# Optimization experiments

Measured on AMD Instinct MI355X. Metric: run time of the kernel, lower is better.

The kernel has to match this reference:

```python
import jax, jax.numpy as jnp
import numpy as np

EPS = 1e-5

def _bn(x, gamma, beta):
    # BatchNorm1d forward (batch statistics, biased variance) over node dim
    mu = x.mean(axis=0)
    var = x.var(axis=0)
    return gamma * (x - mu) * jax.lax.rsqrt(var + EPS) + beta

def _gcn_conv(x, W, b, src, dst, n):
    # PyG GCNConv: h = x @ W; symmetric norm with self-loops; scatter-add to dst
    h = x @ W                                   # [N, out]
    ones = jnp.ones(src.shape, dtype=h.dtype)
    deg = jax.ops.segment_sum(ones, dst, num_segments=n) + 1.0  # +1 self-loop
    dinv = jax.lax.rsqrt(deg)                   # deg >= 1 always
    norm = dinv[src] * dinv[dst]                # [E]
    agg = jax.ops.segment_sum(h[src] * norm[:, None], dst, num_segments=n)
    agg = agg + h * (dinv * dinv)[:, None]      # self-loop contribution
    return agg + b

def setup_inputs() -> dict:
    key = jax.random.key(0)
    ks = jax.random.split(key, 10)
    N, E = 100000, 1600000
    Din, Dh, Dout = 256, 128, 128
    e_prev = jax.random.normal(ks[0], (N, Din), dtype=jnp.float32)
    edge_index = jax.random.randint(ks[1], (2, E), 0, N, dtype=jnp.int64)
    proj_W = jax.random.normal(ks[2], (Din, Din), dtype=jnp.float32) * 0.02
    proj_b = jnp.zeros((Din,), dtype=jnp.float32)
    W1 = jax.random.normal(ks[3], (Din, Dh), dtype=jnp.float32) * 0.05
    b1 = jnp.zeros((Dh,), dtype=jnp.float32)
    gamma1 = jnp.ones((Dh,), dtype=jnp.float32)
    beta1 = jnp.zeros((Dh,), dtype=jnp.float32)
    W2 = jax.random.normal(ks[4], (Dh, Dout), dtype=jnp.float32) * 0.05
    b2 = jnp.zeros((Dout,), dtype=jnp.float32)
    gamma2 = jnp.ones((Dout,), dtype=jnp.float32)
    beta2 = jnp.zeros((Dout,), dtype=jnp.float32)
    return {"e_prev": e_prev, "edge_index": edge_index,
            "proj_W": proj_W, "proj_b": proj_b,
            "W1": W1, "b1": b1, "gamma1": gamma1, "beta1": beta1,
            "W2": W2, "b2": b2, "gamma2": gamma2, "beta2": beta2}

def reference(e_prev, edge_index, proj_W, proj_b, W1, b1, gamma1, beta1, W2, b2, gamma2, beta2):
    n = e_prev.shape[0]
    src, dst = edge_index[0], edge_index[1]
    # input_projection (input_dim != hidden_dim branch)
    x = e_prev @ proj_W + proj_b
    x = _gcn_conv(x, W1, b1, src, dst, n)
    x = _bn(x, gamma1, beta1)
    x = jax.nn.relu(x)
    # dropout(0.2) is identity in eval mode
    x = _gcn_conv(x, W2, b2, src, dst, n)
    x = _bn(x, gamma2, beta2)
    return x
```

## Files before the change

### kernel.cpp

```cpp
#include <hip/hip_runtime.h>
#include <hip/hip_bf16.h>
#include <math.h>

#define BN_EPS 1e-5f
#define CAP 6144
#define MAXB 512

typedef __attribute__((ext_vector_type(8))) short short8;
typedef __attribute__((ext_vector_type(4))) float floatx4;

__global__ void init_kernel(int* __restrict__ bcursor, float* __restrict__ stats, int nb) {
    int i = threadIdx.x + blockIdx.x * blockDim.x;
    if (i < nb) bcursor[i] = i * CAP;
    if (i < 1536) stats[i] = 0.0f;
}

__global__ __launch_bounds__(256) void bucket_kernel(
    const int* __restrict__ src, const int* __restrict__ dst,
    int* __restrict__ bcursor, unsigned* __restrict__ buck, int E, int nb)
{
    __shared__ int h[MAXB], resv[MAXB], cur[MAXB];
    for (int t = threadIdx.x; t < nb; t += 256) { h[t] = 0; cur[t] = 0; }
    __syncthreads();
    int per = (E + gridDim.x - 1) / gridDim.x;
    int e0 = blockIdx.x * per;
    int e1 = min(e0 + per, E);
    for (int e = e0 + threadIdx.x; e < e1; e += 256) {
        int d = __builtin_nontemporal_load(&dst[e]);
        atomicAdd(&h[d >> 8], 1);
    }
    __syncthreads();
    for (int t = threadIdx.x; t < nb; t += 256) {
        int c = h[t];
        if (c > 0) resv[t] = atomicAdd(&bcursor[t], c);
    }
    __syncthreads();
    for (int e = e0 + threadIdx.x; e < e1; e += 256) {
        int d = __builtin_nontemporal_load(&dst[e]);
        int s = __builtin_nontemporal_load(&src[e]);
        int b = d >> 8;
        int pos = resv[b] + atomicAdd(&cur[b], 1);
        buck[pos] = ((unsigned)(d & 255) << 17) | (unsigned)s;
    }
}

__global__ void scanB_kernel(const int* __restrict__ bcursor, int* __restrict__ csrBase, int nb) {
    if (threadIdx.x == 0) {
        int run = 0;
        for (int b = 0; b < nb; ++b) {
            csrBase[b] = run;
            run += bcursor[b] - b * CAP;
        }
        csrBase[nb] = run;
    }
}

__global__ __launch_bounds__(256) void csr_kernel(
    const unsigned* __restrict__ buck, const int* __restrict__ bcursor,
    const int* __restrict__ csrBase,
    int* __restrict__ cnt, int* __restrict__ rowptr, float* __restrict__ dinv,
    int* __restrict__ ssrc, int N)
{
    __shared__ int h[256], sc[256], lcur[256];
    int b = blockIdx.x;
    int t = threadIdx.x;
    h[t] = 0;
    __syncthreads();
    int base = b * CAP;
    int nB = bcursor[b] - base;
    for (int i = t; i < nB; i += 256) {
        unsigned v = buck[base + i];
        atomicAdd(&h[v >> 17], 1);
    }
    __syncthreads();
    int myc = h[t];
    sc[t] = myc;
    __syncthreads();
    for (int off = 1; off < 256; off <<= 1) {
        int x = (t >= off) ? sc[t - off] : 0;
        __syncthreads();
        sc[t] += x;
        __syncthreads();
    }
    int ex = sc[t] - myc;
    lcur[t] = ex;
    int node = b * 256 + t;
    int cb = csrBase[b];
    if (node < N) {
        cnt[node]    = myc;
        rowptr[node] = cb + ex;
        dinv[node]   = rsqrtf((float)myc + 1.0f);
    }
    __syncthreads();
    for (int i = t; i < nB; i += 256) {
        unsigned v = buck[base + i];
        int dloc = v >> 17;
        int pos = cb + atomicAdd(&lcur[dloc], 1);
        ssrc[pos] = (int)(v & 0x1FFFFu);
    }
}

__global__ void wcpack_kernel(const float* __restrict__ PW, const float* __restrict__ W1,
                              const float* __restrict__ pb,
                              __hip_bfloat16* __restrict__ Wf1, float* __restrict__ bc) {
    int c = threadIdx.x;
    if (blockIdx.x == 256) {
        float acc = 0.f;
        for (int k = 0; k < 256; ++k) acc = fmaf(pb[k], W1[k * 128 + c], acc);
        bc[c] = acc;
        return;
    }
    int k = blockIdx.x;
    float acc = 0.f;
    for (int kk = 0; kk < 256; ++kk) acc = fmaf(PW[k * 256 + kk], W1[kk * 128 + c], acc);
    int kc = k >> 5, r5 = k & 31, qq = r5 >> 3, j = r5 & 7;
    int ct = c >> 4, l16 = c & 15;
    int lane = qq * 16 + l16;
    Wf1[(((kc * 8 + ct) * 64) + lane) * 8 + j] = __float2bfloat16(acc);
}

template <int K>
__global__ void packW_kernel(const float* __restrict__ W, __hip_bfloat16* __restrict__ Wf) {
    int t = blockIdx.x * 256 + threadIdx.x;
    if (t >= (K / 32) * 8 * 64 * 8) return;
    int j    = t & 7;
    int lane = (t >> 3) & 63;
    int ct   = (t >> 9) & 7;
    int kc   = t >> 12;
    int k = kc * 32 + ((lane >> 4) & 3) * 8 + j;
    int c = ct * 16 + (lane & 15);
    Wf[t] = __float2bfloat16(W[k * 128 + c]);
}

__device__ inline short8 cvt8(float4 a, float4 b) {
    __hip_bfloat162 p0 = __float22bfloat162_rn(make_float2(a.x, a.y));
    __hip_bfloat162 p1 = __float22bfloat162_rn(make_float2(a.z, a.w));
    __hip_bfloat162 p2 = __float22bfloat162_rn(make_float2(b.x, b.y));
    __hip_bfloat162 p3 = __float22bfloat162_rn(make_float2(b.z, b.w));
    union { short8 s; __hip_bfloat162 h[4]; } u;
    u.h[0] = p0; u.h[1] = p1; u.h[2] = p2; u.h[3] = p3;
    return u.s;
}

template <int K, bool BN>
__global__ __launch_bounds__(256) void mfma_gemm(
    const float* __restrict__ X, const short* __restrict__ Wf,
    const float* __restrict__ bias, const float* __restrict__ dinv,
    const float* __restrict__ scale, const float* __restrict__ shift,
    __hip_bfloat16* __restrict__ Hs, int N)
{
    const int wave = threadIdx.x >> 6;
    const int lane = threadIdx.x & 63;
    const int l16  = lane & 15;
    const int q    = lane >> 4;
    const int r0   = blockIdx.x * 128 + wave * 32;

    const int ra0 = min(r0 + l16, N - 1);
    const int ra1 = min(r0 + 16 + l16, N - 1);
    const float* pA0 = X + (size_t)ra0 * K + q * 8;
    const float* pA1 = X + (size_t)ra1 * K + q * 8;
    const short8* WF = (const short8*)Wf;

    floatx4 acc[2][8];
#pragma unroll
    for (int rt = 0; rt < 2; ++rt)
#pragma unroll
        for (int ct = 0; ct < 8; ++ct) { acc[rt][ct][0] = 0.f; acc[rt][ct][1] = 0.f; acc[rt][ct][2] = 0.f; acc[rt][ct][3] = 0.f; }

#pragma unroll
    for (int kc = 0; kc < K / 32; ++kc) {
        short8 b[8];
#pragma unroll
        for (int ct = 0; ct < 8; ++ct) b[ct] = WF[(kc * 8 + ct) * 64 + lane];

        float4 x00 = *(const float4*)(pA0 + kc * 32);
        float4 x01 = *(const float4*)(pA0 + kc * 32 + 4);
        float4 x10 = *(const float4*)(pA1 + kc * 32);
        float4 x11 = *(const float4*)(pA1 + kc * 32 + 4);
        if (BN) {
            float4 sc0 = *(const float4*)(scale + kc * 32 + q * 8);
            float4 sc1 = *(const float4*)(scale + kc * 32 + q * 8 + 4);
            float4 sh0 = *(const float4*)(shift + kc * 32 + q * 8);
            float4 sh1 = *(const float4*)(shift + kc * 32 + q * 8 + 4);
            x00.x = fmaxf(fmaf(x00.x, sc0.x, sh0.x), 0.f);
            x00.y = fmaxf(fmaf(x00.y, sc0.y, sh0.y), 0.f);
            x00.z = fmaxf(fmaf(x00.z, sc0.z, sh0.z), 0.f);
            x00.w = fmaxf(fmaf(x00.w, sc0.w, sh0.w), 0.f);
            x01.x = fmaxf(fmaf(x01.x, sc1.x, sh1.x), 0.f);
            x01.y = fmaxf(fmaf(x01.y, sc1.y, sh1.y), 0.f);
            x01.z = fmaxf(fmaf(x01.z, sc1.z, sh1.z), 0.f);
            x01.w = fmaxf(fmaf(x01.w, sc1.w, sh1.w), 0.f);
            x10.x = fmaxf(fmaf(x10.x, sc0.x, sh0.x), 0.f);
            x10.y = fmaxf(fmaf(x10.y, sc0.y, sh0.y), 0.f);
            x10.z = fmaxf(fmaf(x10.z, sc0.z, sh0.z), 0.f);
            x10.w = fmaxf(fmaf(x10.w, sc0.w, sh0.w), 0.f);
            x11.x = fmaxf(fmaf(x11.x, sc1.x, sh1.x), 0.f);
            x11.y = fmaxf(fmaf(x11.y, sc1.y, sh1.y), 0.f);
            x11.z = fmaxf(fmaf(x11.z, sc1.z, sh1.z), 0.f);
            x11.w = fmaxf(fmaf(x11.w, sc1.w, sh1.w), 0.f);
        }
        short8 a0 = cvt8(x00, x01);
        short8 a1 = cvt8(x10, x11);
#pragma unroll
        for (int ct = 0; ct < 8; ++ct) {
            acc[0][ct] = __builtin_amdgcn_mfma_f32_16x16x32_bf16(a0, b[ct], acc[0][ct], 0, 0, 0);
            acc[1][ct] = __builtin_amdgcn_mfma_f32_16x16x32_bf16(a1, b[ct], acc[1][ct], 0, 0, 0);
        }
    }

    float bb[8];
#pragma unroll
    for (int ct = 0; ct < 8; ++ct) bb[ct] = bias ? bias[ct * 16 + l16] : 0.f;

#pragma unroll
    for (int rt = 0; rt < 2; ++rt) {
        int rbase = r0 + rt * 16 + q * 4;
        float dv[4];
#pragma unroll
        for (int i = 0; i < 4; ++i) dv[i] = dinv[min(rbase + i, N - 1)];
#pragma unroll
        for (int ct = 0; ct < 8; ++ct) {
#pragma unroll
            for (int i = 0; i < 4; ++i) {
                int row = rbase + i;
                if (row < N)
                    Hs[(size_t)row * 128 + ct * 16 + l16] =
                        __float2bfloat16((acc[rt][ct][i] + bb[ct]) * dv[i]);
            }
        }
    }
}

__device__ inline void acc2(uint2 u, float& x0, float& x1, float& x2, float& x3) {
    x0 += __uint_as_float(u.x << 16);
    x1 += __uint_as_float(u.x & 0xffff0000u);
    x2 += __uint_as_float(u.y << 16);
    x3 += __uint_as_float(u.y & 0xffff0000u);
}

__global__ __launch_bounds__(256) void agg_gather_kernel(
    const uint2* __restrict__ Hu, const int* __restrict__ rowptr,
    const int* __restrict__ cnt, const int* __restrict__ ssrc,
    const float* __restrict__ dinv, const float* __restrict__ bias,
    float* __restrict__ Out, int N)
{
    int node = blockIdx.x * 4 + (threadIdx.x >> 6);
    if (node >= N) return;
    int lane = threadIdx.x & 63;
    int half = lane >> 5;
    int l32  = lane & 31;
    size_t rsel = (size_t)node * 32 + l32;

    float a0 = 0.f, a1 = 0.f, a2 = 0.f, a3 = 0.f;
    float b0 = 0.f, b1 = 0.f, b2 = 0.f, b3 = 0.f;
    float c0 = 0.f, c1 = 0.f, c2 = 0.f, c3 = 0.f;
    float d0 = 0.f, d1 = 0.f, d2 = 0.f, d3 = 0.f;

    if (half == 0) acc2(Hu[rsel], a0, a1, a2, a3);

    int start = rowptr[node];
    int num   = cnt[node];
    int j = 0;
    for (; j + 8 <= num; j += 8) {
        int e = start + j + half;
        int s0 = ssrc[e];
        int s1 = ssrc[e + 2];
        int s2 = ssrc[e + 4];
        int s3 = ssrc[e + 6];
        uint2 u0 = Hu[(size_t)s0 * 32 + l32];
        uint2 u1 = Hu[(size_t)s1 * 32 + l32];
        uint2 u2 = Hu[(size_t)s2 * 32 + l32];
        uint2 u3 = Hu[(size_t)s3 * 32 + l32];
        acc2(u0, a0, a1, a2, a3);
        acc2(u1, b0, b1, b2, b3);
        acc2(u2, c0, c1, c2, c3);
        acc2(u3, d0, d1, d2, d3);
    }
    for (; j + 2 <= num; j += 2) {
        int s = ssrc[start + j + half];
        acc2(Hu[(size_t)s * 32 + l32], a0, a1, a2, a3);
    }
    if (half == 0 && j < num) {
        int s = ssrc[start + j];
        acc2(Hu[(size_t)s * 32 + l32], b0, b1, b2, b3);
    }

    a0 += b0 + c0 + d0;
    a1 += b1 + c1 + d1;
    a2 += b2 + c2 + d2;
    a3 += b3 + c3 + d3;
    a0 += __shfl_xor(a0, 32, 64);
    a1 += __shfl_xor(a1, 32, 64);
    a2 += __shfl_xor(a2, 32, 64);
    a3 += __shfl_xor(a3, 32, 64);

    if (half == 0) {
        float di = dinv[node];
        float4 bb = ((const float4*)bias)[l32];
        float4 o;
        o.x = fmaf(a0, di, bb.x);
        o.y = fmaf(a1, di, bb.y);
        o.z = fmaf(a2, di, bb.z);
        o.w = fmaf(a3, di, bb.w);
        ((float4*)Out)[rsel] = o;
    }
}

__global__ __launch_bounds__(256) void bn_stats_kernel(
    const float* __restrict__ A, float* __restrict__ sum, float* __restrict__ sq, int N)
{
    int c    = threadIdx.x & 127;
    int half = threadIdx.x >> 7;
    int r0   = blockIdx.x * 512;
    float s = 0.f, s2 = 0.f;
    for (int j = half; j < 512; j += 2) {
        int r = r0 + j;
        if (r < N) {
            float v = A[(size_t)r * 128 + c];
            s += v;
            s2 += v * v;
        }
    }
    __shared__ float ls[256], ls2[256];
    ls[threadIdx.x] = s;
    ls2[threadIdx.x] = s2;
    __syncthreads();
    if (threadIdx.x < 128) {
        float ts = ls[threadIdx.x] + ls[threadIdx.x + 128];
        float t2 = ls2[threadIdx.x] + ls2[threadIdx.x + 128];
        __hip_atomic_fetch_add(&sum[c], ts, __ATOMIC_RELAXED, __HIP_MEMORY_SCOPE_AGENT);
        __hip_atomic_fetch_add(&sq[c],  t2, __ATOMIC_RELAXED, __HIP_MEMORY_SCOPE_AGENT);
    }
}

__global__ void bn_final_kernel(const float* __restrict__ sum, const float* __restrict__ sq,
                                float* __restrict__ mu, float* __restrict__ rstd,
                                const float* __restrict__ gamma, const float* __restrict__ beta,
                                float* __restrict__ scale, float* __restrict__ shift, int N) {
    int c = threadIdx.x;
    if (c < 128) {
        float m = sum[c] / (float)N;
        float v = sq[c] / (float)N - m * m;
        float rs = rsqrtf(v + BN_EPS);
        mu[c] = m;
        rstd[c] = rs;
        if (scale) {
            float sc = gamma[c] * rs;
            scale[c] = sc;
            shift[c] = fmaf(-m, sc, beta[c]);
        }
    }
}

__global__ void bn_apply_kernel(float* __restrict__ A, const float* __restrict__ gamma,
                                const float* __restrict__ beta, const float* __restrict__ mu,
                                const float* __restrict__ rstd, int N) {
    int i = blockIdx.x * blockDim.x + threadIdx.x;
    if (i >= N * 32) return;
    int c4 = i & 31;
    float4 v  = ((float4*)A)[i];
    float4 g  = ((const float4*)gamma)[c4];
    float4 b  = ((const float4*)beta)[c4];
    float4 m  = ((const float4*)mu)[c4];
    float4 rs = ((const float4*)rstd)[c4];
    v.x = fmaf(g.x * (v.x - m.x), rs.x, b.x);
    v.y = fmaf(g.y * (v.y - m.y), rs.y, b.y);
    v.z = fmaf(g.z * (v.z - m.z), rs.z, b.z);
    v.w = fmaf(g.w * (v.w - m.w), rs.w, b.w);
    ((float4*)A)[i] = v;
}

extern "C" void kernel_launch(void* const* d_in, const int* in_sizes, int n_in,
                              void* d_out, int out_size, void* d_ws, size_t ws_size,
                              hipStream_t stream) {
    const float* e_prev = (const float*)d_in[0];
    const int*   edges  = (const int*)d_in[1];
    const float* proj_W = (const float*)d_in[2];
    const float* proj_b = (const float*)d_in[3];
    const float* W1     = (const float*)d_in[4];
    const float* b1     = (const float*)d_in[5];
    const float* gamma1 = (const float*)d_in[6];
    const float* beta1  = (const float*)d_in[7];
    const float* W2     = (const float*)d_in[8];
    const float* b2     = (const float*)d_in[9];
    const float* gamma2 = (const float*)d_in[10];
    const float* beta2  = (const float*)d_in[11];
    float* out = (float*)d_out;

    const int N = in_sizes[0] / 256;
    const int E = in_sizes[1] / 2;
    const int* src = edges;
    const int* dst = edges + E;
    const int nb = (N + 255) >> 8;

    char* p = (char*)d_ws;
    const size_t NH = (size_t)N * 128;
    __hip_bfloat16* Hs = (__hip_bfloat16*)p;  p += NH * 2;
    unsigned* buck  = (unsigned*)p; p += (size_t)nb * CAP * 4;
    int* ssrc   = (int*)p;  p += (size_t)E * 4;
    int* cnt    = (int*)p;  p += (size_t)N * 4;
    int* rowptr = (int*)p;  p += (size_t)N * 4;
    float* dinv = (float*)p; p += (size_t)N * 4;
    int* bcursor = (int*)p; p += (size_t)(nb + 16) * 4;
    int* csrBase = (int*)p; p += (size_t)(nb + 16) * 4;
    float* bc   = (float*)p; p += 128 * 4;
    float* stats = (float*)p; p += 1536 * 4;
    __hip_bfloat16* Wf1 = (__hip_bfloat16*)p; p += 256 * 128 * 2;
    __hip_bfloat16* Wf2 = (__hip_bfloat16*)p; p += 128 * 128 * 2;
    float* sum1 = stats,       *sq1 = stats + 128, *mu1 = stats + 256, *rs1 = stats + 384;
    float* sum2 = stats + 512, *sq2 = stats + 640, *mu2 = stats + 768, *rs2 = stats + 896;
    float* scale1 = stats + 1024, *shift1 = stats + 1152;

    init_kernel<<<(1536 + 255) / 256, 256, 0, stream>>>(bcursor, stats, nb);
    bucket_kernel<<<512, 256, 0, stream>>>(src, dst, bcursor, buck, E, nb);
    scanB_kernel<<<1, 64, 0, stream>>>(bcursor, csrBase, nb);
    csr_kernel<<<nb, 256, 0, stream>>>(buck, bcursor, csrBase, cnt, rowptr, dinv, ssrc, N);

    wcpack_kernel<<<257, 128, 0, stream>>>(proj_W, W1, proj_b, Wf1, bc);
    packW_kernel<128><<<(128 * 128 + 255) / 256, 256, 0, stream>>>(W2, Wf2);

    const int gemm_grid = (N + 127) / 128;

    mfma_gemm<256, false><<<gemm_grid, 256, 0, stream>>>(
        e_prev, (const short*)Wf1, bc, dinv, nullptr, nullptr, Hs, N);
    agg_gather_kernel<<<(N + 3) / 4, 256, 0, stream>>>(
        (const uint2*)Hs, rowptr, cnt, ssrc, dinv, b1, out, N);
    bn_stats_kernel<<<(N + 511) / 512, 256, 0, stream>>>(out, sum1, sq1, N);
    bn_final_kernel<<<1, 128, 0, stream>>>(sum1, sq1, mu1, rs1, gamma1, beta1, scale1, shift1, N);

    mfma_gemm<128, true><<<gemm_grid, 256, 0, stream>>>(
        out, (const short*)Wf2, nullptr, dinv, scale1, shift1, Hs, N);
    agg_gather_kernel<<<(N + 3) / 4, 256, 0, stream>>>(
        (const uint2*)Hs, rowptr, cnt, ssrc, dinv, b2, out, N);
    bn_stats_kernel<<<(N + 511) / 512, 256, 0, stream>>>(out, sum2, sq2, N);
    bn_final_kernel<<<1, 128, 0, stream>>>(sum2, sq2, mu2, rs2, nullptr, nullptr, nullptr, nullptr, N);
    bn_apply_kernel<<<(N * 32 + 255) / 256, 256, 0, stream>>>(out, gamma2, beta2, mu2, rs2, N);
}
```

Measured before the change: 642.4 us.

## Parallelize bucket scan, use nontemporal memory ops, replace BN atomics with partial sums

Replaces the single-thread bucket prefix scan with a 512-thread shared-memory scan. Adds nontemporal hints to streaming loads (bucket entries, GEMM inputs, edge sources) and to the output stores of gather and BN apply. Rewrites the BN statistics kernel to use float4 loads and per-block partial sums that the finalize kernel reduces, removing global float atomics and the stats zeroing. Nontemporal stores may hurt if the next kernel rereads the data from L2.

```diff
diff --git a/kernel.cpp b/kernel.cpp
--- a/kernel.cpp
+++ b/kernel.cpp
@@ -8,11 +8,16 @@
 
 typedef __attribute__((ext_vector_type(8))) short short8;
 typedef __attribute__((ext_vector_type(4))) float floatx4;
-
-__global__ void init_kernel(int* __restrict__ bcursor, float* __restrict__ stats, int nb) {
+typedef __attribute__((ext_vector_type(2))) unsigned uvec2;
+
+__device__ inline float4 ntload4(const float* p) {
+    floatx4 v = __builtin_nontemporal_load((const floatx4*)p);
+    return make_float4(v.x, v.y, v.z, v.w);
+}
+
+__global__ void init_kernel(int* __restrict__ bcursor, int nb) {
     int i = threadIdx.x + blockIdx.x * blockDim.x;
     if (i < nb) bcursor[i] = i * CAP;
-    if (i < 1536) stats[i] = 0.0f;
 }
 
 __global__ __launch_bounds__(256) void bucket_kernel(
@@ -44,15 +49,23 @@
     }
 }
 
-__global__ void scanB_kernel(const int* __restrict__ bcursor, int* __restrict__ csrBase, int nb) {
-    if (threadIdx.x == 0) {
-        int run = 0;
-        for (int b = 0; b < nb; ++b) {
-            csrBase[b] = run;
-            run += bcursor[b] - b * CAP;
-        }
-        csrBase[nb] = run;
-    }
+__global__ __launch_bounds__(512) void scanB_kernel(
+    const int* __restrict__ bcursor, int* __restrict__ csrBase, int nb)
+{
+    __shared__ int sc[512];
+    int t = threadIdx.x;
+    int v = (t < nb) ? (bcursor[t] - t * CAP) : 0;
+    sc[t] = v;
+    __syncthreads();
+    for (int off = 1; off < 512; off <<= 1) {
+        int x = (t >= off) ? sc[t - off] : 0;
+        __syncthreads();
+        sc[t] += x;
+        __syncthreads();
+    }
+    if (t < nb) csrBase[t] = sc[t] - v;
+    if (t == nb) csrBase[nb] = sc[nb - 1 < 0 ? 0 : nb - 1];
+    if (t == 511 && nb <= 511) csrBase[nb] = sc[nb - 1];
 }
 
 __global__ __launch_bounds__(256) void csr_kernel(
@@ -69,7 +82,7 @@
     int base = b * CAP;
     int nB = bcursor[b] - base;
     for (int i = t; i < nB; i += 256) {
-        unsigned v = buck[base + i];
+        unsigned v = __builtin_nontemporal_load(&buck[base + i]);
         atomicAdd(&h[v >> 17], 1);
     }
     __syncthreads();
@@ -93,7 +106,7 @@
     }
     __syncthreads();
     for (int i = t; i < nB; i += 256) {
-        unsigned v = buck[base + i];
+        unsigned v = __builtin_nontemporal_load(&buck[base + i]);
         int dloc = v >> 17;
         int pos = cb + atomicAdd(&lcur[dloc], 1);
         ssrc[pos] = (int)(v & 0x1FFFFu);
@@ -173,10 +186,10 @@
 #pragma unroll
         for (int ct = 0; ct < 8; ++ct) b[ct] = WF[(kc * 8 + ct) * 64 + lane];
 
-        float4 x00 = *(const float4*)(pA0 + kc * 32);
-        float4 x01 = *(const float4*)(pA0 + kc * 32 + 4);
-        float4 x10 = *(const float4*)(pA1 + kc * 32);
-        float4 x11 = *(const float4*)(pA1 + kc * 32 + 4);
+        float4 x00 = ntload4(pA0 + kc * 32);
+        float4 x01 = ntload4(pA0 + kc * 32 + 4);
+        float4 x10 = ntload4(pA1 + kc * 32);
+        float4 x11 = ntload4(pA1 + kc * 32 + 4);
         if (BN) {
             float4 sc0 = *(const float4*)(scale + kc * 32 + q * 8);
             float4 sc1 = *(const float4*)(scale + kc * 32 + q * 8 + 4);
@@ -263,10 +276,10 @@
     int j = 0;
     for (; j + 8 <= num; j += 8) {
         int e = start + j + half;
-        int s0 = ssrc[e];
-        int s1 = ssrc[e + 2];
-        int s2 = ssrc[e + 4];
-        int s3 = ssrc[e + 6];
+        int s0 = __builtin_nontemporal_load(&ssrc[e]);
+        int s1 = __builtin_nontemporal_load(&ssrc[e + 2]);
+        int s2 = __builtin_nontemporal_load(&ssrc[e + 4]);
+        int s3 = __builtin_nontemporal_load(&ssrc[e + 6]);
         uint2 u0 = Hu[(size_t)s0 * 32 + l32];
         uint2 u1 = Hu[(size_t)s1 * 32 + l32];
         uint2 u2 = Hu[(size_t)s2 * 32 + l32];
@@ -277,11 +290,11 @@
         acc2(u3, d0, d1, d2, d3);
     }
     for (; j + 2 <= num; j += 2) {
-        int s = ssrc[start + j + half];
+        int s = __builtin_nontemporal_load(&ssrc[start + j + half]);
         acc2(Hu[(size_t)s * 32 + l32], a0, a1, a2, a3);
     }
     if (half == 0 && j < num) {
-        int s = ssrc[start + j];
+        int s = __builtin_nontemporal_load(&ssrc[start + j]);
         acc2(Hu[(size_t)s * 32 + l32], b0, b1, b2, b3);
     }
 
@@ -297,50 +310,66 @@
     if (half == 0) {
         float di = dinv[node];
         float4 bb = ((const float4*)bias)[l32];
-        float4 o;
-        o.x = fmaf(a0, di, bb.x);
-        o.y = fmaf(a1, di, bb.y);
-        o.z = fmaf(a2, di, bb.z);
-        o.w = fmaf(a3, di, bb.w);
-        ((float4*)Out)[rsel] = o;
+        floatx4 o;
+        o[0] = fmaf(a0, di, bb.x);
+        o[1] = fmaf(a1, di, bb.y);
+        o[2] = fmaf(a2, di, bb.z);
+        o[3] = fmaf(a3, di, bb.w);
+        __builtin_nontemporal_store(o, (floatx4*)Out + rsel);
     }
 }
 
 __global__ __launch_bounds__(256) void bn_stats_kernel(
-    const float* __restrict__ A, float* __restrict__ sum, float* __restrict__ sq, int N)
-{
-    int c    = threadIdx.x & 127;
-    int half = threadIdx.x >> 7;
-    int r0   = blockIdx.x * 512;
-    float s = 0.f, s2 = 0.f;
-    for (int j = half; j < 512; j += 2) {
-        int r = r0 + j;
-        if (r < N) {
-            float v = A[(size_t)r * 128 + c];
-            s += v;
-            s2 += v * v;
-        }
-    }
-    __shared__ float ls[256], ls2[256];
+    const float* __restrict__ A, float* __restrict__ partS, float* __restrict__ partQ,
+    int N, int R)
+{
+    int col4   = threadIdx.x & 31;
+    int rowoff = threadIdx.x >> 5;
+    int r0 = blockIdx.x * R;
+    int r1 = min(r0 + R, N);
+    float4 s = make_float4(0.f, 0.f, 0.f, 0.f);
+    float4 qq = make_float4(0.f, 0.f, 0.f, 0.f);
+#pragma unroll 4
+    for (int r = r0 + rowoff; r < r1; r += 8) {
+        float4 v = *(const float4*)&A[(size_t)r * 128 + col4 * 4];
+        s.x += v.x; s.y += v.y; s.z += v.z; s.w += v.w;
+        qq.x = fmaf(v.x, v.x, qq.x);
+        qq.y = fmaf(v.y, v.y, qq.y);
+        qq.z = fmaf(v.z, v.z, qq.z);
+        qq.w = fmaf(v.w, v.w, qq.w);
+    }
+    __shared__ float4 ls[256], lq[256];
     ls[threadIdx.x] = s;
-    ls2[threadIdx.x] = s2;
-    __syncthreads();
-    if (threadIdx.x < 128) {
-        float ts = ls[threadIdx.x] + ls[threadIdx.x + 128];
-        float t2 = ls2[threadIdx.x] + ls2[threadIdx.x + 128];
-        __hip_atomic_fetch_add(&sum[c], ts, __ATOMIC_RELAXED, __HIP_MEMORY_SCOPE_AGENT);
-        __hip_atomic_fetch_add(&sq[c],  t2, __ATOMIC_RELAXED, __HIP_MEMORY_SCOPE_AGENT);
-    }
-}
-
-__global__ void bn_final_kernel(const float* __restrict__ sum, const float* __restrict__ sq,
+    lq[threadIdx.x] = qq;
+    __syncthreads();
+    if (threadIdx.x < 32) {
+        float4 ts = ls[threadIdx.x], tq = lq[threadIdx.x];
+#pragma unroll
+        for (int k = 1; k < 8; ++k) {
+            float4 xs = ls[k * 32 + threadIdx.x];
+            float4 xq = lq[k * 32 + threadIdx.x];
+            ts.x += xs.x; ts.y += xs.y; ts.z += xs.z; ts.w += xs.w;
+            tq.x += xq.x; tq.y += xq.y; tq.z += xq.z; tq.w += xq.w;
+        }
+        *(float4*)&partS[(size_t)blockIdx.x * 128 + threadIdx.x * 4] = ts;
+        *(float4*)&partQ[(size_t)blockIdx.x * 128 + threadIdx.x * 4] = tq;
+    }
+}
+
+__global__ void bn_final_kernel(const float* __restrict__ partS, const float* __restrict__ partQ,
+                                int npart,
                                 float* __restrict__ mu, float* __restrict__ rstd,
                                 const float* __restrict__ gamma, const float* __restrict__ beta,
                                 float* __restrict__ scale, float* __restrict__ shift, int N) {
     int c = threadIdx.x;
     if (c < 128) {
-        float m = sum[c] / (float)N;
-        float v = sq[c] / (float)N - m * m;
+        float s = 0.f, q = 0.f;
+        for (int b = 0; b < npart; ++b) {
+            s += partS[(size_t)b * 128 + c];
+            q += partQ[(size_t)b * 128 + c];
+        }
+        float m = s / (float)N;
+        float v = q / (float)N - m * m;
         float rs = rsqrtf(v + BN_EPS);
         mu[c] = m;
         rstd[c] = rs;
@@ -363,11 +392,12 @@
     float4 b  = ((const float4*)beta)[c4];
     float4 m  = ((const float4*)mu)[c4];
     float4 rs = ((const float4*)rstd)[c4];
-    v.x = fmaf(g.x * (v.x - m.x), rs.x, b.x);
-    v.y = fmaf(g.y * (v.y - m.y), rs.y, b.y);
-    v.z = fmaf(g.z * (v.z - m.z), rs.z, b.z);
-    v.w = fmaf(g.w * (v.w - m.w), rs.w, b.w);
-    ((float4*)A)[i] = v;
+    floatx4 o;
+    o[0] = fmaf(g.x * (v.x - m.x), rs.x, b.x);
+    o[1] = fmaf(g.y * (v.y - m.y), rs.y, b.y);
+    o[2] = fmaf(g.z * (v.z - m.z), rs.z, b.z);
+    o[3] = fmaf(g.w * (v.w - m.w), rs.w, b.w);
+    __builtin_nontemporal_store(o, (floatx4*)A + i);
 }
 
 extern "C" void kernel_launch(void* const* d_in, const int* in_sizes, int n_in,
@@ -392,6 +422,7 @@
     const int* src = edges;
     const int* dst = edges + E;
     const int nb = (N + 255) >> 8;
+    const int R = (N + 255) / 256;
 
     char* p = (char*)d_ws;
     const size_t NH = (size_t)N * 128;
@@ -405,15 +436,17 @@
     int* csrBase = (int*)p; p += (size_t)(nb + 16) * 4;
     float* bc   = (float*)p; p += 128 * 4;
     float* stats = (float*)p; p += 1536 * 4;
+    float* partS = (float*)p; p += 256 * 128 * 4;
+    float* partQ = (float*)p; p += 256 * 128 * 4;
     __hip_bfloat16* Wf1 = (__hip_bfloat16*)p; p += 256 * 128 * 2;
     __hip_bfloat16* Wf2 = (__hip_bfloat16*)p; p += 128 * 128 * 2;
-    float* sum1 = stats,       *sq1 = stats + 128, *mu1 = stats + 256, *rs1 = stats + 384;
-    float* sum2 = stats + 512, *sq2 = stats + 640, *mu2 = stats + 768, *rs2 = stats + 896;
+    float* mu1 = stats + 256, *rs1 = stats + 384;
+    float* mu2 = stats + 768, *rs2 = stats + 896;
     float* scale1 = stats + 1024, *shift1 = stats + 1152;
 
-    init_kernel<<<(1536 + 255) / 256, 256, 0, stream>>>(bcursor, stats, nb);
+    init_kernel<<<(nb + 255) / 256, 256, 0, stream>>>(bcursor, nb);
     bucket_kernel<<<512, 256, 0, stream>>>(src, dst, bcursor, buck, E, nb);
-    scanB_kernel<<<1, 64, 0, stream>>>(bcursor, csrBase, nb);
+    scanB_kernel<<<1, 512, 0, stream>>>(bcursor, csrBase, nb);
     csr_kernel<<<nb, 256, 0, stream>>>(buck, bcursor, csrBase, cnt, rowptr, dinv, ssrc, N);
 
     wcpack_kernel<<<257, 128, 0, stream>>>(proj_W, W1, proj_b, Wf1, bc);
@@ -425,14 +458,16 @@
         e_prev, (const short*)Wf1, bc, dinv, nullptr, nullptr, Hs, N);
     agg_gather_kernel<<<(N + 3) / 4, 256, 0, stream>>>(
         (const uint2*)Hs, rowptr, cnt, ssrc, dinv, b1, out, N);
-    bn_stats_kernel<<<(N + 511) / 512, 256, 0, stream>>>(out, sum1, sq1, N);
-    bn_final_kernel<<<1, 128, 0, stream>>>(sum1, sq1, mu1, rs1, gamma1, beta1, scale1, shift1, N);
+    bn_stats_kernel<<<256, 256, 0, stream>>>(out, partS, partQ, N, R);
+    bn_final_kernel<<<1, 128, 0, stream>>>(partS, partQ, 256, mu1, rs1,
+                                           gamma1, beta1, scale1, shift1, N);
 
     mfma_gemm<128, true><<<gemm_grid, 256, 0, stream>>>(
         out, (const short*)Wf2, nullptr, dinv, scale1, shift1, Hs, N);
     agg_gather_kernel<<<(N + 3) / 4, 256, 0, stream>>>(
         (const uint2*)Hs, rowptr, cnt, ssrc, dinv, b2, out, N);
-    bn_stats_kernel<<<(N + 511) / 512, 256, 0, stream>>>(out, sum2, sq2, N);
-    bn_final_kernel<<<1, 128, 0, stream>>>(sum2, sq2, mu2, rs2, nullptr, nullptr, nullptr, nullptr, N);
+    bn_stats_kernel<<<256, 256, 0, stream>>>(out, partS, partQ, N, R);
+    bn_final_kernel<<<1, 128, 0, stream>>>(partS, partQ, 256, mu2, rs2,
+                                           nullptr, nullptr, nullptr, nullptr, N);
     bn_apply_kernel<<<(N * 32 + 255) / 256, 256, 0, stream>>>(out, gamma2, beta2, mu2, rs2, N);
 }
```

After: 635.9 us. Within noise of the previous version (-1.0%).
